# Kernel optimization log

Measured on AMD Instinct MI355X. Metric: run time of the kernel, lower is better.

The kernel has to match this reference:

```python
import jax, jax.numpy as jnp
import numpy as np

H = 768; NH = 8; DH = H // NH; MAXLEN = 512; EPS = 1e-5

def _sinusoid_pe():
    # get_embedding(max_seq_len, hidden, rel_pos_init=0): rows 0..2*max_len
    num = 2 * MAXLEN + 1
    half = H // 2
    inv = np.exp(np.arange(half, dtype=np.float64) * -(np.log(10000.0) / (half - 1)))
    ang = np.arange(num, dtype=np.float64)[:, None] * inv[None, :]
    return jnp.asarray(np.concatenate([np.sin(ang), np.cos(ang)], axis=1), jnp.float32)

def setup_inputs():
    key = jax.random.key(0)
    ks = jax.random.split(key, 20)
    B, S = 2, 192
    p = lambda k, shp: jax.random.normal(k, shp, jnp.float32) * 0.02
    z = lambda *shp: jnp.zeros(shp, jnp.float32)
    o = lambda *shp: jnp.ones(shp, jnp.float32)
    return dict(
        word_embedding=jax.random.normal(ks[0], (B, S, H), jnp.float32),
        bert_embedding=jax.random.normal(ks[1], (B, S, H), jnp.float32),
        seq_len=jax.random.randint(ks[2], (B,), 128, 161),
        lex_num=jax.random.randint(ks[3], (B,), 16, 32),
        pos_s=jax.random.randint(ks[4], (B, S), 0, 192),
        pos_e=jax.random.randint(ks[5], (B, S), 0, 192),
        pe=_sinusoid_pe(),
        Wf1=p(ks[6], (4 * H, 4 * H)), bf1=z(4 * H),
        Wf2=p(ks[7], (4 * H, 4)), bf2=z(4),
        Wq=p(ks[8], (H, H)), bq=z(H),
        Wk=p(ks[9], (H, H)), bk=z(H),
        Wv=p(ks[10], (H, H)), bv=z(H),
        Wr=p(ks[11], (H, H)), br=z(H),
        u=p(ks[12], (NH, DH)), v=p(ks[13], (NH, DH)),
        Wo=p(ks[14], (H, H)), bo=z(H),
        ln1_g=o(H), ln1_b=z(H),
        W1=p(ks[15], (H, H)), b1=z(H),
        W2=p(ks[16], (H, H)), b2=z(H),
        ln2_g=o(H), ln2_b=z(H),
    )

def _ln(x, g, b):
    m = jnp.mean(x, -1, keepdims=True)
    var = jnp.mean((x - m) ** 2, -1, keepdims=True)
    return (x - m) * jax.lax.rsqrt(var + EPS) * g + b

def reference(word_embedding, bert_embedding, seq_len, lex_num, pos_s, pos_e, pe,
              Wf1, bf1, Wf2, bf2, Wq, bq, Wk, bk, Wv, bv, Wr, br, u, v, Wo, bo,
              ln1_g, ln1_b, W1, b1, W2, b2, ln2_g, ln2_b):
    B, S, _ = word_embedding.shape
    x = bert_embedding + word_embedding  # [B,S,H]
    # --- four-way relative position fusion ('attn') ---
    dss = pos_s[:, :, None] - pos_s[:, None, :] + MAXLEN  # [B,S,S] in [0,2*MAXLEN]
    dse = pos_s[:, :, None] - pos_e[:, None, :] + MAXLEN
    des = pos_e[:, :, None] - pos_s[:, None, :] + MAXLEN
    dee = pos_e[:, :, None] - pos_e[:, None, :] + MAXLEN
    pe4 = jnp.concatenate([pe[dss], pe[dse], pe[des], pe[dee]], axis=-1)  # [B,S,S,4H]
    w4 = jax.nn.softmax(jax.nn.relu(pe4 @ Wf1 + bf1) @ Wf2 + bf2, axis=-1)  # [B,S,S,4]
    rel = jnp.einsum('bqkf,bqkfh->bqkh', w4, pe4.reshape(B, S, S, 4, H))  # [B,S,S,H]
    # --- lattice relative multi-head attention (Transformer-XL style A+C / B+D) ---
    q = (x @ Wq + bq).reshape(B, S, NH, DH)
    k = (x @ Wk + bk).reshape(B, S, NH, DH)
    vh = (x @ Wv + bv).reshape(B, S, NH, DH)
    r = (rel @ Wr + br).reshape(B, S, S, NH, DH)
    AC = jnp.einsum('bqnd,bknd->bnqk', q + u, k)
    BD = jnp.einsum('bqnd,bqknd->bnqk', q + v, r)
    att = (AC + BD) / np.sqrt(DH).astype(np.float32)  # scaled=True
    valid = jnp.arange(S)[None, :] < (seq_len + lex_num)[:, None]  # [B,S] key mask
    att = jnp.where(valid[:, None, None, :], att, jnp.float32(-1e15))
    pattn = jax.nn.softmax(att, axis=-1)
    ctx = jnp.einsum('bnqk,bknd->bqnd', pattn, vh).reshape(B, S, H)
    ctx = ctx @ Wo + bo  # attn_ff=True
    x = _ln(x + ctx, ln1_g, ln1_b)  # postprocess 'an'
    ff = jax.nn.relu(x @ W1 + b1) @ W2 + b2  # ff_size = hidden
    x = _ln(x + ff, ln2_g, ln2_b)
    return x[:, :256, :]
```

## Files before the change

kernel.cpp:

```cpp
#include <hip/hip_runtime.h>
#include <hip/hip_bf16.h>
#include <hip/hip_fp16.h>
#include <cstdint>

#define BB 2
#define SS 192
#define HH 768
#define NHH 8
#define DHH 96
#define H4 3072
#define NJ 383
#define NJP 384
#define JOFF 321
#define NPAIR 73728
#define ATT_SCALE 0.10206207261596575f

typedef _Float16 h2 __attribute__((ext_vector_type(2)));
typedef _Float16 h4v __attribute__((ext_vector_type(4)));
typedef _Float16 h8 __attribute__((ext_vector_type(8)));
typedef float f4 __attribute__((ext_vector_type(4)));

__global__ __launch_bounds__(256) void prep_kernel(
    const float4* __restrict__ we, const float4* __restrict__ be, float4* __restrict__ xb,
    const float* __restrict__ wf2, const float* __restrict__ bf1,
    const float* __restrict__ bq, const float* __restrict__ bk, const float* __restrict__ bv,
    h2* __restrict__ wf2pG, h2* __restrict__ bf1pG, float* __restrict__ bqkv,
    const float* __restrict__ s0, const float* __restrict__ s1, const float* __restrict__ s2,
    const float* __restrict__ s3, const float* __restrict__ s4, const float* __restrict__ s5,
    const float* __restrict__ s6, __half* __restrict__ BTsq,
    const float* __restrict__ Wf1, __half* __restrict__ BTf1) {
  __shared__ float tile[32][33];
  const int blk = blockIdx.x;
  const int t = threadIdx.x;
  if (blk < 288) {
    const int i = blk * 256 + t;
    float4 va = we[i], vb = be[i];
    xb[i] = make_float4(va.x + vb.x, va.y + vb.y, va.z + vb.z, va.w + vb.w);
  } else if (blk == 288) {
    for (int i = t; i < 6144; i += 256) {
      const int cw = i >> 2, f = i & 3;
      h2 v = {(_Float16)wf2[8 * cw + f], (_Float16)wf2[8 * cw + 4 + f]};
      wf2pG[i] = v;
    }
    for (int i = t; i < 1536; i += 256) {
      h2 v = {(_Float16)bf1[2 * i], (_Float16)bf1[2 * i + 1]};
      bf1pG[i] = v;
    }
    for (int i = t; i < 768; i += 256) {
      bqkv[i] = bq[i]; bqkv[768 + i] = bk[i]; bqkv[1536 + i] = bv[i];
    }
  } else if (blk < 4321) {
    const int i7 = blk - 289;
    const int z = i7 / 576, rem = i7 % 576;
    const int y = (rem / 24) * 32, x = (rem % 24) * 32;
    const float* src;
    switch (z) {
      case 0: src = s0; break; case 1: src = s1; break; case 2: src = s2; break;
      case 3: src = s3; break; case 4: src = s4; break; case 5: src = s5; break;
      default: src = s6; break;
    }
    __half* dst = BTsq + (size_t)z * HH * HH;
    const int tx = t & 31, ty = t >> 5;
#pragma unroll
    for (int i = 0; i < 4; ++i)
      tile[ty + 8 * i][tx] = src[(size_t)(y + ty + 8 * i) * HH + x + tx];
    __syncthreads();
#pragma unroll
    for (int i = 0; i < 4; ++i)
      dst[(size_t)(x + ty + 8 * i) * HH + y + tx] = __float2half(tile[tx][ty + 8 * i]);
  } else {
    const int ic = blk - 4321;
    const int z = ic / 2304, rem = ic % 2304;
    const int y = (rem / 96) * 32, x = (rem % 96) * 32;
    const float* src = Wf1 + (size_t)z * HH * H4;
    __half* dst = BTf1 + (size_t)z * HH * H4;
    const int tx = t & 31, ty = t >> 5;
#pragma unroll
    for (int i = 0; i < 4; ++i)
      tile[ty + 8 * i][tx] = src[(size_t)(y + ty + 8 * i) * H4 + x + tx];
    __syncthreads();
#pragma unroll
    for (int i = 0; i < 4; ++i)
      dst[(size_t)(x + ty + 8 * i) * HH + y + tx] = __float2half(tile[tx][ty + 8 * i]);
  }
}

template<bool OUT_HALF, bool RELU>
__device__ __forceinline__ void gemm_body(_Float16 (*As)[72], _Float16 (*Bs)[72],
    const float* __restrict__ A, const __half* __restrict__ Bb, const float* __restrict__ bias,
    void* __restrict__ Cv, int M, int N, int K, int bm, int bn, int t) {
  const int wave = t >> 6, lane = t & 63;
  const int wr = (wave >> 1) * 64, wc = (wave & 1) * 64;
  const int lrow = lane & 15, khalf = lane >> 4;
  const int arow = t >> 4, acol = (t & 15) << 2;
  const int brow = t >> 3, bcol = (t & 7) << 3;
  f4 acc[4][4] = {};
  const int nk = K >> 6;
  float4 ra[8]; h8 rb[4];

#define LOAD_TILE(kt) { \
  _Pragma("unroll") for (int i = 0; i < 8; ++i) { \
    const int row = arow + (i << 4); \
    if (bm + row < M) ra[i] = *(const float4*)(A + (size_t)(bm + row) * K + (size_t)(kt) * 64 + acol); \
    else ra[i] = make_float4(0.f, 0.f, 0.f, 0.f); } \
  _Pragma("unroll") for (int i = 0; i < 4; ++i) { \
    const int row = brow + (i << 5); \
    rb[i] = *(const h8*)(Bb + (size_t)(bn + row) * K + (size_t)(kt) * 64 + bcol); } }

#define STORE_TILE() { \
  _Pragma("unroll") for (int i = 0; i < 8; ++i) { \
    const int row = arow + (i << 4); \
    h4v hv = {(_Float16)ra[i].x, (_Float16)ra[i].y, (_Float16)ra[i].z, (_Float16)ra[i].w}; \
    *(h4v*)&As[row][acol] = hv; } \
  _Pragma("unroll") for (int i = 0; i < 4; ++i) { \
    const int row = brow + (i << 5); \
    *(h8*)&Bs[row][bcol] = rb[i]; } }

  LOAD_TILE(0)
  STORE_TILE()
  __syncthreads();
  for (int kt = 0; kt < nk; ++kt) {
    const bool more = (kt + 1 < nk);
    if (more) { LOAD_TILE(kt + 1) }
#pragma unroll
    for (int ks = 0; ks < 2; ++ks) {
      h8 af[4], bf[4];
#pragma unroll
      for (int mi = 0; mi < 4; ++mi) af[mi] = *(const h8*)&As[wr + mi * 16 + lrow][ks * 32 + (khalf << 3)];
#pragma unroll
      for (int ni = 0; ni < 4; ++ni) bf[ni] = *(const h8*)&Bs[wc + ni * 16 + lrow][ks * 32 + (khalf << 3)];
#pragma unroll
      for (int mi = 0; mi < 4; ++mi)
#pragma unroll
        for (int ni = 0; ni < 4; ++ni)
          acc[mi][ni] = __builtin_amdgcn_mfma_f32_16x16x32_f16(af[mi], bf[ni], acc[mi][ni], 0, 0, 0);
    }
    __syncthreads();
    if (more) { STORE_TILE() }
    __syncthreads();
  }
#undef LOAD_TILE
#undef STORE_TILE
  const int crow0 = (lane >> 4) << 2;
  const int ccol = lane & 15;
#pragma unroll
  for (int mi = 0; mi < 4; ++mi) {
#pragma unroll
    for (int r = 0; r < 4; ++r) {
      const int row = bm + wr + mi * 16 + crow0 + r;
      if (row >= M) continue;
#pragma unroll
      for (int ni = 0; ni < 4; ++ni) {
        const int col = bn + wc + ni * 16 + ccol;
        float v = acc[mi][ni][r];
        if (bias) v += bias[col];
        if (RELU) v = fmaxf(v, 0.f);
        if (OUT_HALF) ((__half*)Cv)[(size_t)row * N + col] = __float2half(v);
        else          ((float*)Cv)[(size_t)row * N + col] = v;
      }
    }
  }
}

template<bool OUT_HALF, bool RELU>
__global__ __launch_bounds__(256) void mfma_gemm(const float* __restrict__ A,
    const __half* __restrict__ BT, const float* __restrict__ bias, void* __restrict__ Cv,
    int M, int N, int K) {
  __shared__ _Float16 As[128][72];
  __shared__ _Float16 Bs[128][72];
  gemm_body<OUT_HALF, RELU>(As, Bs, A, BT, bias, Cv, M, N, K,
                            blockIdx.y * 128, blockIdx.x * 128, threadIdx.x);
}

__global__ __launch_bounds__(256) void gemm_batch(
    const float* __restrict__ peu, const __half* __restrict__ WrT, const float* __restrict__ br,
    float* __restrict__ PRb,
    const __half* __restrict__ BTf1, __half* __restrict__ Tt,
    const float* __restrict__ xb, const __half* __restrict__ BTsq, const float* __restrict__ bqkv,
    float* __restrict__ qkv) {
  __shared__ _Float16 As[128][72];
  __shared__ _Float16 Bs[128][72];
  const int blk = blockIdx.x;
  const int t = threadIdx.x;
  if (blk < 18) {
    gemm_body<false, false>(As, Bs, peu, WrT, br, PRb, NJ, HH, HH,
                            (blk / 6) * 128, (blk % 6) * 128, t);
  } else if (blk < 306) {
    const int i2 = blk - 18;
    const int z = i2 / 72, r = i2 % 72;
    gemm_body<true, false>(As, Bs, peu, BTf1 + (size_t)z * H4 * HH, nullptr,
                           Tt + (size_t)z * NJP * H4, NJ, H4, HH,
                           (r / 24) * 128, (r % 24) * 128, t);
  } else {
    const int i3 = blk - 306;
    gemm_body<false, false>(As, Bs, xb, BTsq, bqkv, qkv, BB * SS, 3 * HH, HH,
                            (i3 / 18) * 128, (i3 % 18) * 128, t);
  }
}

__global__ __launch_bounds__(256) void g2_kernel(const float* __restrict__ qkv,
    const float* __restrict__ PRb, const float* __restrict__ vv, float* __restrict__ G) {
  __shared__ float Qv[192][100];
  __shared__ float PRs[48][100];
  const int blk = blockIdx.x;
  const int jt = blk & 7, n = (blk >> 3) & 7, b = blk >> 6;
  const int j0 = jt * 48;
  const int t = threadIdx.x;
  for (int i = t; i < 4608; i += 256) {
    const int q = i / 24, c = (i % 24) * 4;
    float4 v = *(const float4*)(qkv + (size_t)(b * 192 + q) * 2304 + n * 96 + c);
    const float4 vb = *(const float4*)(vv + n * 96 + c);
    Qv[q][c] = v.x + vb.x; Qv[q][c + 1] = v.y + vb.y;
    Qv[q][c + 2] = v.z + vb.z; Qv[q][c + 3] = v.w + vb.w;
  }
  for (int i = t; i < 1152; i += 256) {
    const int jr = i / 24, c = (i % 24) * 4;
    const int j = min(j0 + jr, NJ - 1);
    *(f4*)&PRs[jr][c] = *(const f4*)(PRb + (size_t)j * 768 + n * 96 + c);
  }
  __syncthreads();
  const int qt = t >> 4, jt2 = t & 15;
  const int qb0 = qt * 12;
  float acc[12][3] = {};
  for (int dq = 0; dq < 24; ++dq) {
    const f4 p0 = *(const f4*)&PRs[jt2][dq * 4];
    const f4 p1 = *(const f4*)&PRs[jt2 + 16][dq * 4];
    const f4 p2 = *(const f4*)&PRs[jt2 + 32][dq * 4];
#pragma unroll
    for (int qi = 0; qi < 12; ++qi) {
      const f4 qv = *(const f4*)&Qv[qb0 + qi][dq * 4];
      acc[qi][0] += qv.x * p0.x + qv.y * p0.y + qv.z * p0.z + qv.w * p0.w;
      acc[qi][1] += qv.x * p1.x + qv.y * p1.y + qv.z * p1.z + qv.w * p1.w;
      acc[qi][2] += qv.x * p2.x + qv.y * p2.y + qv.z * p2.z + qv.w * p2.w;
    }
  }
  float* Grow = G + (size_t)(b * 8 + n) * 192 * NJP;
#pragma unroll
  for (int qi = 0; qi < 12; ++qi)
#pragma unroll
    for (int ji = 0; ji < 3; ++ji)
      Grow[(size_t)(qb0 + qi) * NJP + j0 + jt2 + 16 * ji] = acc[qi][ji];
}

__global__ __launch_bounds__(256) void pairA_kernel(const h2* __restrict__ Tt,
    const h8* __restrict__ wf2pG, const h2* __restrict__ bf1pG,
    const int* __restrict__ pos_s, const int* __restrict__ pos_e,
    float* __restrict__ partials) {
  const int blk = blockIdx.x;
  const int chunk = (blk & 7) >> 1;
  const int cbase = chunk * 384;
  const int t = threadIdx.x;
  const int grp = t >> 4, l16 = t & 15;
  const int pbase = (blk >> 3) * 128 + (blk & 1) * 64;
  const h2 zero2 = {(_Float16)0.f, (_Float16)0.f};
  h8 Wr[3][4]; h2 B1[3][4];
#pragma unroll
  for (int s = 0; s < 3; ++s)
#pragma unroll
    for (int v = 0; v < 4; ++v) {
      const int cw = (l16 + 16 * s) * 4 + v;
      Wr[s][v] = wf2pG[cbase + cw];
      B1[s][v] = bf1pG[cbase + cw];
    }
  const h2* Tc = Tt + cbase;
#pragma unroll 2
  for (int i = 0; i < 4; ++i) {
    const int p = pbase + i * 16 + grp;
    const int b = p / 36864;
    const int rem = p - b * 36864;
    const int qq = rem / 192;
    const int kk = rem - qq * 192;
    const int psq = pos_s[b * 192 + qq], peq = pos_e[b * 192 + qq];
    const int psk = pos_s[b * 192 + kk], pek = pos_e[b * 192 + kk];
    const int jx = min(max(psq - psk + 191, 0), NJ - 1);
    const int jy = min(max(psq - pek + 191, 0), NJ - 1);
    const int jz = min(max(peq - psk + 191, 0), NJ - 1);
    const int jw = min(max(peq - pek + 191, 0), NJ - 1);
    const h8* r0 = (const h8*)(Tc + (size_t)jx * 1536);
    const h8* r1 = (const h8*)(Tc + (size_t)(NJP + jy) * 1536);
    const h8* r2 = (const h8*)(Tc + (size_t)(2 * NJP + jz) * 1536);
    const h8* r3 = (const h8*)(Tc + (size_t)(3 * NJP + jw) * 1536);
    h2 c0 = zero2, c1 = zero2, c2 = zero2, c3 = zero2;
#pragma unroll
    for (int s = 0; s < 3; ++s) {
      const int g = l16 + 16 * s;
      union { h8 v; h2 p[4]; } L0, L1, L2, L3;
      L0.v = r0[g]; L1.v = r1[g]; L2.v = r2[g]; L3.v = r3[g];
#pragma unroll
      for (int v = 0; v < 4; ++v) {
        h2 sv = L0.p[v] + L1.p[v];
        sv = sv + L2.p[v];
        sv = sv + L3.p[v];
        sv = sv + B1[s][v];
        sv = __builtin_elementwise_max(sv, zero2);
        union { h8 v; h2 p[4]; } W; W.v = Wr[s][v];
        c0 += sv * W.p[0];
        c1 += sv * W.p[1];
        c2 += sv * W.p[2];
        c3 += sv * W.p[3];
      }
    }
    float a0 = (float)c0.x + (float)c0.y;
    float a1 = (float)c1.x + (float)c1.y;
    float a2 = (float)c2.x + (float)c2.y;
    float a3 = (float)c3.x + (float)c3.y;
#pragma unroll
    for (int off = 8; off > 0; off >>= 1) {
      a0 += __shfl_xor(a0, off, 16);
      a1 += __shfl_xor(a1, off, 16);
      a2 += __shfl_xor(a2, off, 16);
      a3 += __shfl_xor(a3, off, 16);
    }
    if (l16 < 4) {
      const float sel = (l16 == 0) ? a0 : (l16 == 1) ? a1 : (l16 == 2) ? a2 : a3;
      partials[((size_t)chunk * NPAIR + p) * 4 + l16] = sel;
    }
  }
}

__global__ __launch_bounds__(256) void attn2_kernel(const float* __restrict__ qkv,
    const float* __restrict__ uu, const float* __restrict__ G,
    const float4* __restrict__ parti4, const float* __restrict__ bf2,
    const int* __restrict__ pos_s, const int* __restrict__ pos_e,
    const int* __restrict__ seq_len, const int* __restrict__ lex_num,
    __half* __restrict__ P) {
  __shared__ float Ks[192][100];
  __shared__ float Qs[12][100];
  __shared__ float Gs[12][388];
  __shared__ int poss[192], pose[192];
  const int blk = blockIdx.x;
  const int qt = blk & 15, n = (blk >> 4) & 7, b = blk >> 7;
  const int q0 = qt * 12;
  const int t = threadIdx.x;
  for (int i = t; i < 4608; i += 256) {
    const int k = i / 24, c = (i % 24) * 4;
    *(f4*)&Ks[k][c] = *(const f4*)(qkv + (size_t)(b * 192 + k) * 2304 + 768 + n * 96 + c);
  }
  for (int i = t; i < 288; i += 256) {
    const int qi = i / 24, c = (i % 24) * 4;
    float4 v = *(const float4*)(qkv + (size_t)(b * 192 + q0 + qi) * 2304 + n * 96 + c);
    const float4 ub = *(const float4*)(uu + n * 96 + c);
    Qs[qi][c] = v.x + ub.x; Qs[qi][c + 1] = v.y + ub.y;
    Qs[qi][c + 2] = v.z + ub.z; Qs[qi][c + 3] = v.w + ub.w;
  }
  for (int i = t; i < 1152; i += 256) {
    const int qi = i / 96, c = (i % 96) * 4;
    *(f4*)&Gs[qi][c] = *(const f4*)(G + ((size_t)(b * 8 + n) * 192 + q0 + qi) * NJP + c);
  }
  for (int i = t; i < 192; i += 256) { poss[i] = pos_s[b * 192 + i]; pose[i] = pos_e[b * 192 + i]; }
  __syncthreads();
  const float b20 = bf2[0], b21 = bf2[1], b22 = bf2[2], b23 = bf2[3];
  const int wave = t >> 6, lane = t & 63;
  const int qw = wave * 3;
  float ac[3][3] = {};
  for (int dq = 0; dq < 24; ++dq) {
    const f4 kv0 = *(const f4*)&Ks[lane][dq * 4];
    const f4 kv1 = *(const f4*)&Ks[lane + 64][dq * 4];
    const f4 kv2 = *(const f4*)&Ks[lane + 128][dq * 4];
#pragma unroll
    for (int qi = 0; qi < 3; ++qi) {
      const f4 qv = *(const f4*)&Qs[qw + qi][dq * 4];
      ac[qi][0] += qv.x * kv0.x + qv.y * kv0.y + qv.z * kv0.z + qv.w * kv0.w;
      ac[qi][1] += qv.x * kv1.x + qv.y * kv1.y + qv.z * kv1.z + qv.w * kv1.w;
      ac[qi][2] += qv.x * kv2.x + qv.y * kv2.y + qv.z * kv2.z + qv.w * kv2.w;
    }
  }
  const int vbnd = seq_len[b] + lex_num[b];
#pragma unroll
  for (int qi = 0; qi < 3; ++qi) {
    const int qg = q0 + qw + qi;
    const int psq = poss[qg], peq = pose[qg];
    float v[3];
#pragma unroll
    for (int ki = 0; ki < 3; ++ki) {
      const int k = lane + 64 * ki;
      const int psk = poss[k], pek = pose[k];
      const int jss = min(max(psq - psk + 191, 0), NJ - 1);
      const int jse = min(max(psq - pek + 191, 0), NJ - 1);
      const int jes = min(max(peq - psk + 191, 0), NJ - 1);
      const int jee = min(max(peq - pek + 191, 0), NJ - 1);
      const int pidx = b * 36864 + qg * 192 + k;
      const float4 s0 = parti4[pidx];
      const float4 s1 = parti4[NPAIR + pidx];
      const float4 s2 = parti4[2 * NPAIR + pidx];
      const float4 s3 = parti4[3 * NPAIR + pidx];
      const float l0 = s0.x + s1.x + s2.x + s3.x + b20;
      const float l1 = s0.y + s1.y + s2.y + s3.y + b21;
      const float l2 = s0.z + s1.z + s2.z + s3.z + b22;
      const float l3 = s0.w + s1.w + s2.w + s3.w + b23;
      const float lm = fmaxf(fmaxf(l0, l1), fmaxf(l2, l3));
      const float e0 = __expf(l0 - lm), e1 = __expf(l1 - lm);
      const float e2 = __expf(l2 - lm), e3 = __expf(l3 - lm);
      const float winv = 1.f / (e0 + e1 + e2 + e3);
      const float bd = (e0 * Gs[qw + qi][jss] + e1 * Gs[qw + qi][jse]
                      + e2 * Gs[qw + qi][jes] + e3 * Gs[qw + qi][jee]) * winv;
      const float a = (ac[qi][ki] + bd) * ATT_SCALE;
      v[ki] = (k < vbnd) ? a : -1e15f;
    }
    float mx = fmaxf(fmaxf(v[0], v[1]), v[2]);
#pragma unroll
    for (int off = 1; off < 64; off <<= 1) mx = fmaxf(mx, __shfl_xor(mx, off, 64));
    const float e0 = __expf(v[0] - mx), e1 = __expf(v[1] - mx), e2 = __expf(v[2] - mx);
    float sm = e0 + e1 + e2;
#pragma unroll
    for (int off = 1; off < 64; off <<= 1) sm += __shfl_xor(sm, off, 64);
    const float inv = 1.f / sm;
    __half* pr = P + ((size_t)(b * 8 + n) * 192 + qg) * 192;
    pr[lane] = __float2half(e0 * inv);
    pr[lane + 64] = __float2half(e1 * inv);
    pr[lane + 128] = __float2half(e2 * inv);
  }
}

__global__ __launch_bounds__(256) void ctx2_kernel(const __half* __restrict__ P,
    const float* __restrict__ qkv, float* __restrict__ ctx) {
  __shared__ float Vs[192][100];
  __shared__ float Ps[48][196];
  const int blk = blockIdx.x;
  const int qt = blk & 3, n = (blk >> 2) & 7, b = blk >> 5;
  const int q0 = qt * 48;
  const int t = threadIdx.x;
  for (int i = t; i < 4608; i += 256) {
    const int k = i / 24, c = (i % 24) * 4;
    *(f4*)&Vs[k][c] = *(const f4*)(qkv + (size_t)(b * 192 + k) * 2304 + 1536 + n * 96 + c);
  }
  const __half* Pb = P + ((size_t)(b * 8 + n) * 192 + q0) * 192;
  for (int i = t; i < 4608; i += 256) {
    const int qi = i / 96, c = (i % 96) * 2;
    const h2 pv = *(const h2*)(Pb + (size_t)qi * 192 + c);
    Ps[qi][c] = (float)pv.x; Ps[qi][c + 1] = (float)pv.y;
  }
  __syncthreads();
  const int qt2 = t >> 5, dt = t & 31;
  const int qb0 = qt2 * 6;
  float acc[6][3] = {};
  for (int k4 = 0; k4 < 48; ++k4) {
    const int k = k4 * 4;
    f4 pq[6];
#pragma unroll
    for (int qi = 0; qi < 6; ++qi) pq[qi] = *(const f4*)&Ps[qb0 + qi][k];
#pragma unroll
    for (int kk = 0; kk < 4; ++kk) {
      const float v0 = Vs[k + kk][dt];
      const float v1 = Vs[k + kk][dt + 32];
      const float v2 = Vs[k + kk][dt + 64];
#pragma unroll
      for (int qi = 0; qi < 6; ++qi) {
        const float pv = pq[qi][kk];
        acc[qi][0] += pv * v0; acc[qi][1] += pv * v1; acc[qi][2] += pv * v2;
      }
    }
  }
#pragma unroll
  for (int qi = 0; qi < 6; ++qi) {
    float* cr = ctx + (size_t)(b * 192 + q0 + qb0 + qi) * 768 + n * 96;
    cr[dt] = acc[qi][0]; cr[dt + 32] = acc[qi][1]; cr[dt + 64] = acc[qi][2];
  }
}

__global__ __launch_bounds__(256) void ln_kernel(const float* __restrict__ xin,
    const float* __restrict__ dres, const float* __restrict__ g,
    const float* __restrict__ bta, float* __restrict__ out) {
  const int row = blockIdx.x;
  const int t = threadIdx.x;
  __shared__ float red[256];
  const size_t base = (size_t)row * HH;
  const float v0 = xin[base + t] + dres[base + t];
  const float v1 = xin[base + 256 + t] + dres[base + 256 + t];
  const float v2 = xin[base + 512 + t] + dres[base + 512 + t];
  red[t] = v0 + v1 + v2; __syncthreads();
  for (int s = 128; s > 0; s >>= 1) { if (t < s) red[t] += red[t + s]; __syncthreads(); }
  const float mean = red[0] * (1.f / 768.f); __syncthreads();
  red[t] = v0 * v0 + v1 * v1 + v2 * v2; __syncthreads();
  for (int s = 128; s > 0; s >>= 1) { if (t < s) red[t] += red[t + s]; __syncthreads(); }
  const float var = red[0] * (1.f / 768.f) - mean * mean;
  const float rstd = rsqrtf(var + 1e-5f);
  out[base + t]       = (v0 - mean) * rstd * g[t]       + bta[t];
  out[base + 256 + t] = (v1 - mean) * rstd * g[256 + t] + bta[256 + t];
  out[base + 512 + t] = (v2 - mean) * rstd * g[512 + t] + bta[512 + t];
}

extern "C" void kernel_launch(void* const* d_in, const int* in_sizes, int n_in,
                              void* d_out, int out_size, void* d_ws, size_t ws_size,
                              hipStream_t stream) {
  const float* we      = (const float*)d_in[0];
  const float* be      = (const float*)d_in[1];
  const int*   seq_len = (const int*)d_in[2];
  const int*   lex_num = (const int*)d_in[3];
  const int*   pos_s   = (const int*)d_in[4];
  const int*   pos_e   = (const int*)d_in[5];
  const float* pe      = (const float*)d_in[6];
  const float* Wf1     = (const float*)d_in[7];
  const float* bf1     = (const float*)d_in[8];
  const float* Wf2     = (const float*)d_in[9];
  const float* bf2     = (const float*)d_in[10];
  const float* Wq = (const float*)d_in[11]; const float* bq = (const float*)d_in[12];
  const float* Wk = (const float*)d_in[13]; const float* bk = (const float*)d_in[14];
  const float* Wv = (const float*)d_in[15]; const float* bv = (const float*)d_in[16];
  const float* Wr = (const float*)d_in[17]; const float* br = (const float*)d_in[18];
  const float* uu = (const float*)d_in[19]; const float* vv = (const float*)d_in[20];
  const float* Wo = (const float*)d_in[21]; const float* bo = (const float*)d_in[22];
  const float* g1 = (const float*)d_in[23]; const float* be1 = (const float*)d_in[24];
  const float* W1 = (const float*)d_in[25]; const float* b1 = (const float*)d_in[26];
  const float* W2 = (const float*)d_in[27]; const float* b2 = (const float*)d_in[28];
  const float* g2 = (const float*)d_in[29]; const float* be2 = (const float*)d_in[30];

  char* ws = (char*)d_ws;
  float*  xb    = (float*)(ws + 0);
  float*  qkv   = (float*)(ws + 1179648);
  float*  PRb   = (float*)(ws + 4718592);
  __half* Tt    = (__half*)(ws + 5898240);
  __half* BTf1  = (__half*)(ws + 15335424);
  float*  G     = (float*)(ws + 15335424);
  float*  parti = (float*)(ws + 20054016);
  __half* P     = (__half*)(ws + 25952256);
  float*  ctx   = (float*)(ws + 27131904);
  float*  ao    = (float*)(ws + 28311552);
  float*  x1    = (float*)(ws + 29491200);
  float*  ff    = (float*)(ws + 30670848);
  float*  fo    = (float*)(ws + 31850496);
  __half* BTsq  = (__half*)(ws + 34209792);
  h2*     wf2pG = (h2*)(ws + 42467328);
  h2*     bf1pG = (h2*)(ws + 42491904);
  float*  bqkv  = (float*)(ws + 42498048);
  float*  out   = (float*)d_out;

  const float* peu = pe + (size_t)JOFF * HH;
  const size_t SQ = (size_t)HH * HH;
  __half* WoT = BTsq + 3 * SQ; __half* W1T = BTsq + 4 * SQ;
  __half* W2T = BTsq + 5 * SQ; __half* WrT = BTsq + 6 * SQ;

  prep_kernel<<<13537, 256, 0, stream>>>((const float4*)we, (const float4*)be, (float4*)xb,
      Wf2, bf1, bq, bk, bv, wf2pG, bf1pG, bqkv,
      Wq, Wk, Wv, Wo, W1, W2, Wr, BTsq, Wf1, BTf1);
  gemm_batch<<<360, 256, 0, stream>>>(peu, WrT, br, PRb, BTf1, Tt, xb, BTsq, bqkv, qkv);
  g2_kernel<<<128, 256, 0, stream>>>(qkv, PRb, vv, G);
  pairA_kernel<<<4608, 256, 0, stream>>>((const h2*)Tt, (const h8*)wf2pG, bf1pG,
      pos_s, pos_e, parti);
  attn2_kernel<<<256, 256, 0, stream>>>(qkv, uu, G, (const float4*)parti, bf2,
      pos_s, pos_e, seq_len, lex_num, P);
  ctx2_kernel<<<64, 256, 0, stream>>>(P, qkv, ctx);
  mfma_gemm<false, false><<<dim3(6, 3), 256, 0, stream>>>(ctx, WoT, bo, ao, BB * SS, HH, HH);
  ln_kernel<<<BB * SS, 256, 0, stream>>>(xb, ao, g1, be1, x1);
  mfma_gemm<false, true><<<dim3(6, 3), 256, 0, stream>>>(x1, W1T, b1, ff, BB * SS, HH, HH);
  mfma_gemm<false, false><<<dim3(6, 3), 256, 0, stream>>>(ff, W2T, b2, fo, BB * SS, HH, HH);
  ln_kernel<<<BB * SS, 256, 0, stream>>>(x1, fo, g2, be2, out);
}
```

Measured before the change: 405.7 us.

## Widen GEMM blocks to 8 waves and split attention/context kernels finer

```diff
diff --git a/kernel.cpp b/kernel.cpp
--- a/kernel.cpp
+++ b/kernel.cpp
@@ -90,30 +90,30 @@
     const float* __restrict__ A, const __half* __restrict__ Bb, const float* __restrict__ bias,
     void* __restrict__ Cv, int M, int N, int K, int bm, int bn, int t) {
   const int wave = t >> 6, lane = t & 63;
-  const int wr = (wave >> 1) * 64, wc = (wave & 1) * 64;
+  const int wr = (wave >> 2) * 64, wc = (wave & 3) * 32;
   const int lrow = lane & 15, khalf = lane >> 4;
   const int arow = t >> 4, acol = (t & 15) << 2;
   const int brow = t >> 3, bcol = (t & 7) << 3;
-  f4 acc[4][4] = {};
+  f4 acc[4][2] = {};
   const int nk = K >> 6;
-  float4 ra[8]; h8 rb[4];
+  float4 ra[4]; h8 rb[2];
 
 #define LOAD_TILE(kt) { \
-  _Pragma("unroll") for (int i = 0; i < 8; ++i) { \
-    const int row = arow + (i << 4); \
+  _Pragma("unroll") for (int i = 0; i < 4; ++i) { \
+    const int row = arow + (i << 5); \
     if (bm + row < M) ra[i] = *(const float4*)(A + (size_t)(bm + row) * K + (size_t)(kt) * 64 + acol); \
     else ra[i] = make_float4(0.f, 0.f, 0.f, 0.f); } \
+  _Pragma("unroll") for (int i = 0; i < 2; ++i) { \
+    const int row = brow + (i << 6); \
+    rb[i] = *(const h8*)(Bb + (size_t)(bn + row) * K + (size_t)(kt) * 64 + bcol); } }
+
+#define STORE_TILE() { \
   _Pragma("unroll") for (int i = 0; i < 4; ++i) { \
-    const int row = brow + (i << 5); \
-    rb[i] = *(const h8*)(Bb + (size_t)(bn + row) * K + (size_t)(kt) * 64 + bcol); } }
-
-#define STORE_TILE() { \
-  _Pragma("unroll") for (int i = 0; i < 8; ++i) { \
-    const int row = arow + (i << 4); \
+    const int row = arow + (i << 5); \
     h4v hv = {(_Float16)ra[i].x, (_Float16)ra[i].y, (_Float16)ra[i].z, (_Float16)ra[i].w}; \
     *(h4v*)&As[row][acol] = hv; } \
-  _Pragma("unroll") for (int i = 0; i < 4; ++i) { \
-    const int row = brow + (i << 5); \
+  _Pragma("unroll") for (int i = 0; i < 2; ++i) { \
+    const int row = brow + (i << 6); \
     *(h8*)&Bs[row][bcol] = rb[i]; } }
 
   LOAD_TILE(0)
@@ -124,15 +124,15 @@
     if (more) { LOAD_TILE(kt + 1) }
 #pragma unroll
     for (int ks = 0; ks < 2; ++ks) {
-      h8 af[4], bf[4];
+      h8 af[4], bf[2];
 #pragma unroll
       for (int mi = 0; mi < 4; ++mi) af[mi] = *(const h8*)&As[wr + mi * 16 + lrow][ks * 32 + (khalf << 3)];
 #pragma unroll
-      for (int ni = 0; ni < 4; ++ni) bf[ni] = *(const h8*)&Bs[wc + ni * 16 + lrow][ks * 32 + (khalf << 3)];
+      for (int ni = 0; ni < 2; ++ni) bf[ni] = *(const h8*)&Bs[wc + ni * 16 + lrow][ks * 32 + (khalf << 3)];
 #pragma unroll
       for (int mi = 0; mi < 4; ++mi)
 #pragma unroll
-        for (int ni = 0; ni < 4; ++ni)
+        for (int ni = 0; ni < 2; ++ni)
           acc[mi][ni] = __builtin_amdgcn_mfma_f32_16x16x32_f16(af[mi], bf[ni], acc[mi][ni], 0, 0, 0);
     }
     __syncthreads();
@@ -150,7 +150,7 @@
       const int row = bm + wr + mi * 16 + crow0 + r;
       if (row >= M) continue;
 #pragma unroll
-      for (int ni = 0; ni < 4; ++ni) {
+      for (int ni = 0; ni < 2; ++ni) {
         const int col = bn + wc + ni * 16 + ccol;
         float v = acc[mi][ni][r];
         if (bias) v += bias[col];
@@ -163,7 +163,7 @@
 }
 
 template<bool OUT_HALF, bool RELU>
-__global__ __launch_bounds__(256) void mfma_gemm(const float* __restrict__ A,
+__global__ __launch_bounds__(512) void mfma_gemm(const float* __restrict__ A,
     const __half* __restrict__ BT, const float* __restrict__ bias, void* __restrict__ Cv,
     int M, int N, int K) {
   __shared__ _Float16 As[128][72];
@@ -172,7 +172,7 @@
                             blockIdx.y * 128, blockIdx.x * 128, threadIdx.x);
 }
 
-__global__ __launch_bounds__(256) void gemm_batch(
+__global__ __launch_bounds__(512) void gemm_batch(
     const float* __restrict__ peu, const __half* __restrict__ WrT, const float* __restrict__ br,
     float* __restrict__ PRb,
     const __half* __restrict__ BTf1, __half* __restrict__ Tt,
@@ -318,144 +318,129 @@
   }
 }
 
-__global__ __launch_bounds__(256) void attn2_kernel(const float* __restrict__ qkv,
+__global__ __launch_bounds__(384) void attn3_kernel(const float* __restrict__ qkv,
     const float* __restrict__ uu, const float* __restrict__ G,
     const float4* __restrict__ parti4, const float* __restrict__ bf2,
     const int* __restrict__ pos_s, const int* __restrict__ pos_e,
     const int* __restrict__ seq_len, const int* __restrict__ lex_num,
     __half* __restrict__ P) {
-  __shared__ float Ks[192][100];
-  __shared__ float Qs[12][100];
-  __shared__ float Gs[12][388];
+  __shared__ _Float16 Kh[192][100];
+  __shared__ float Qs[6][100];
+  __shared__ float Gs[6][388];
   __shared__ int poss[192], pose[192];
   const int blk = blockIdx.x;
-  const int qt = blk & 15, n = (blk >> 4) & 7, b = blk >> 7;
-  const int q0 = qt * 12;
-  const int t = threadIdx.x;
-  for (int i = t; i < 4608; i += 256) {
+  const int qt = blk & 31, n = (blk >> 5) & 7, b = blk >> 8;
+  const int q0 = qt * 6;
+  const int t = threadIdx.x;
+  for (int i = t; i < 4608; i += 384) {
     const int k = i / 24, c = (i % 24) * 4;
-    *(f4*)&Ks[k][c] = *(const f4*)(qkv + (size_t)(b * 192 + k) * 2304 + 768 + n * 96 + c);
-  }
-  for (int i = t; i < 288; i += 256) {
-    const int qi = i / 24, c = (i % 24) * 4;
+    const float4 v = *(const float4*)(qkv + (size_t)(b * 192 + k) * 2304 + 768 + n * 96 + c);
+    h4v hv = {(_Float16)v.x, (_Float16)v.y, (_Float16)v.z, (_Float16)v.w};
+    *(h4v*)&Kh[k][c] = hv;
+  }
+  if (t < 144) {
+    const int qi = t / 24, c = (t % 24) * 4;
     float4 v = *(const float4*)(qkv + (size_t)(b * 192 + q0 + qi) * 2304 + n * 96 + c);
     const float4 ub = *(const float4*)(uu + n * 96 + c);
     Qs[qi][c] = v.x + ub.x; Qs[qi][c + 1] = v.y + ub.y;
     Qs[qi][c + 2] = v.z + ub.z; Qs[qi][c + 3] = v.w + ub.w;
   }
-  for (int i = t; i < 1152; i += 256) {
+  for (int i = t; i < 576; i += 384) {
     const int qi = i / 96, c = (i % 96) * 4;
     *(f4*)&Gs[qi][c] = *(const f4*)(G + ((size_t)(b * 8 + n) * 192 + q0 + qi) * NJP + c);
   }
-  for (int i = t; i < 192; i += 256) { poss[i] = pos_s[b * 192 + i]; pose[i] = pos_e[b * 192 + i]; }
+  for (int i = t; i < 192; i += 384) { poss[i] = pos_s[b * 192 + i]; pose[i] = pos_e[b * 192 + i]; }
   __syncthreads();
   const float b20 = bf2[0], b21 = bf2[1], b22 = bf2[2], b23 = bf2[3];
   const int wave = t >> 6, lane = t & 63;
-  const int qw = wave * 3;
-  float ac[3][3] = {};
+  float ac0 = 0.f, ac1 = 0.f, ac2 = 0.f;
   for (int dq = 0; dq < 24; ++dq) {
-    const f4 kv0 = *(const f4*)&Ks[lane][dq * 4];
-    const f4 kv1 = *(const f4*)&Ks[lane + 64][dq * 4];
-    const f4 kv2 = *(const f4*)&Ks[lane + 128][dq * 4];
-#pragma unroll
-    for (int qi = 0; qi < 3; ++qi) {
-      const f4 qv = *(const f4*)&Qs[qw + qi][dq * 4];
-      ac[qi][0] += qv.x * kv0.x + qv.y * kv0.y + qv.z * kv0.z + qv.w * kv0.w;
-      ac[qi][1] += qv.x * kv1.x + qv.y * kv1.y + qv.z * kv1.z + qv.w * kv1.w;
-      ac[qi][2] += qv.x * kv2.x + qv.y * kv2.y + qv.z * kv2.z + qv.w * kv2.w;
-    }
+    const f4 qv = *(const f4*)&Qs[wave][dq * 4];
+    const h4v k0 = *(const h4v*)&Kh[lane][dq * 4];
+    const h4v k1 = *(const h4v*)&Kh[lane + 64][dq * 4];
+    const h4v k2 = *(const h4v*)&Kh[lane + 128][dq * 4];
+    ac0 += qv.x * (float)k0.x + qv.y * (float)k0.y + qv.z * (float)k0.z + qv.w * (float)k0.w;
+    ac1 += qv.x * (float)k1.x + qv.y * (float)k1.y + qv.z * (float)k1.z + qv.w * (float)k1.w;
+    ac2 += qv.x * (float)k2.x + qv.y * (float)k2.y + qv.z * (float)k2.z + qv.w * (float)k2.w;
   }
   const int vbnd = seq_len[b] + lex_num[b];
-#pragma unroll
-  for (int qi = 0; qi < 3; ++qi) {
-    const int qg = q0 + qw + qi;
-    const int psq = poss[qg], peq = pose[qg];
-    float v[3];
-#pragma unroll
-    for (int ki = 0; ki < 3; ++ki) {
-      const int k = lane + 64 * ki;
-      const int psk = poss[k], pek = pose[k];
-      const int jss = min(max(psq - psk + 191, 0), NJ - 1);
-      const int jse = min(max(psq - pek + 191, 0), NJ - 1);
-      const int jes = min(max(peq - psk + 191, 0), NJ - 1);
-      const int jee = min(max(peq - pek + 191, 0), NJ - 1);
-      const int pidx = b * 36864 + qg * 192 + k;
-      const float4 s0 = parti4[pidx];
-      const float4 s1 = parti4[NPAIR + pidx];
-      const float4 s2 = parti4[2 * NPAIR + pidx];
-      const float4 s3 = parti4[3 * NPAIR + pidx];
-      const float l0 = s0.x + s1.x + s2.x + s3.x + b20;
-      const float l1 = s0.y + s1.y + s2.y + s3.y + b21;
-      const float l2 = s0.z + s1.z + s2.z + s3.z + b22;
-      const float l3 = s0.w + s1.w + s2.w + s3.w + b23;
-      const float lm = fmaxf(fmaxf(l0, l1), fmaxf(l2, l3));
-      const float e0 = __expf(l0 - lm), e1 = __expf(l1 - lm);
-      const float e2 = __expf(l2 - lm), e3 = __expf(l3 - lm);
-      const float winv = 1.f / (e0 + e1 + e2 + e3);
-      const float bd = (e0 * Gs[qw + qi][jss] + e1 * Gs[qw + qi][jse]
-                      + e2 * Gs[qw + qi][jes] + e3 * Gs[qw + qi][jee]) * winv;
-      const float a = (ac[qi][ki] + bd) * ATT_SCALE;
-      v[ki] = (k < vbnd) ? a : -1e15f;
-    }
-    float mx = fmaxf(fmaxf(v[0], v[1]), v[2]);
-#pragma unroll
-    for (int off = 1; off < 64; off <<= 1) mx = fmaxf(mx, __shfl_xor(mx, off, 64));
-    const float e0 = __expf(v[0] - mx), e1 = __expf(v[1] - mx), e2 = __expf(v[2] - mx);
-    float sm = e0 + e1 + e2;
-#pragma unroll
-    for (int off = 1; off < 64; off <<= 1) sm += __shfl_xor(sm, off, 64);
-    const float inv = 1.f / sm;
-    __half* pr = P + ((size_t)(b * 8 + n) * 192 + qg) * 192;
-    pr[lane] = __float2half(e0 * inv);
-    pr[lane + 64] = __float2half(e1 * inv);
-    pr[lane + 128] = __float2half(e2 * inv);
-  }
-}
-
-__global__ __launch_bounds__(256) void ctx2_kernel(const __half* __restrict__ P,
+  const int qg = q0 + wave;
+  const int psq = poss[qg], peq = pose[qg];
+  float v[3];
+  const float acv[3] = {ac0, ac1, ac2};
+#pragma unroll
+  for (int ki = 0; ki < 3; ++ki) {
+    const int k = lane + 64 * ki;
+    const int psk = poss[k], pek = pose[k];
+    const int jss = min(max(psq - psk + 191, 0), NJ - 1);
+    const int jse = min(max(psq - pek + 191, 0), NJ - 1);
+    const int jes = min(max(peq - psk + 191, 0), NJ - 1);
+    const int jee = min(max(peq - pek + 191, 0), NJ - 1);
+    const int pidx = b * 36864 + qg * 192 + k;
+    const float4 s0 = parti4[pidx];
+    const float4 s1 = parti4[NPAIR + pidx];
+    const float4 s2 = parti4[2 * NPAIR + pidx];
+    const float4 s3 = parti4[3 * NPAIR + pidx];
+    const float l0 = s0.x + s1.x + s2.x + s3.x + b20;
+    const float l1 = s0.y + s1.y + s2.y + s3.y + b21;
+    const float l2 = s0.z + s1.z + s2.z + s3.z + b22;
+    const float l3 = s0.w + s1.w + s2.w + s3.w + b23;
+    const float lm = fmaxf(fmaxf(l0, l1), fmaxf(l2, l3));
+    const float e0 = __expf(l0 - lm), e1 = __expf(l1 - lm);
+    const float e2 = __expf(l2 - lm), e3 = __expf(l3 - lm);
+    const float winv = 1.f / (e0 + e1 + e2 + e3);
+    const float bd = (e0 * Gs[wave][jss] + e1 * Gs[wave][jse]
+                    + e2 * Gs[wave][jes] + e3 * Gs[wave][jee]) * winv;
+    const float a = (acv[ki] + bd) * ATT_SCALE;
+    v[ki] = (k < vbnd) ? a : -1e15f;
+  }
+  float mx = fmaxf(fmaxf(v[0], v[1]), v[2]);
+#pragma unroll
+  for (int off = 1; off < 64; off <<= 1) mx = fmaxf(mx, __shfl_xor(mx, off, 64));
+  const float e0 = __expf(v[0] - mx), e1 = __expf(v[1] - mx), e2 = __expf(v[2] - mx);
+  float sm = e0 + e1 + e2;
+#pragma unroll
+  for (int off = 1; off < 64; off <<= 1) sm += __shfl_xor(sm, off, 64);
+  const float inv = 1.f / sm;
+  __half* pr = P + ((size_t)(b * 8 + n) * 192 + qg) * 192;
+  pr[lane] = __float2half(e0 * inv);
+  pr[lane + 64] = __float2half(e1 * inv);
+  pr[lane + 128] = __float2half(e2 * inv);
+}
+
+__global__ __launch_bounds__(384) void ctx3_kernel(const __half* __restrict__ P,
     const float* __restrict__ qkv, float* __restrict__ ctx) {
-  __shared__ float Vs[192][100];
-  __shared__ float Ps[48][196];
+  __shared__ _Float16 Vh[192][100];
+  __shared__ float Ps[12][192];
   const int blk = blockIdx.x;
-  const int qt = blk & 3, n = (blk >> 2) & 7, b = blk >> 5;
-  const int q0 = qt * 48;
-  const int t = threadIdx.x;
-  for (int i = t; i < 4608; i += 256) {
+  const int qt = blk & 15, n = (blk >> 4) & 7, b = blk >> 7;
+  const int q0 = qt * 12;
+  const int t = threadIdx.x;
+  for (int i = t; i < 4608; i += 384) {
     const int k = i / 24, c = (i % 24) * 4;
-    *(f4*)&Vs[k][c] = *(const f4*)(qkv + (size_t)(b * 192 + k) * 2304 + 1536 + n * 96 + c);
+    const float4 v = *(const float4*)(qkv + (size_t)(b * 192 + k) * 2304 + 1536 + n * 96 + c);
+    h4v hv = {(_Float16)v.x, (_Float16)v.y, (_Float16)v.z, (_Float16)v.w};
+    *(h4v*)&Vh[k][c] = hv;
   }
   const __half* Pb = P + ((size_t)(b * 8 + n) * 192 + q0) * 192;
-  for (int i = t; i < 4608; i += 256) {
+  for (int i = t; i < 1152; i += 384) {
     const int qi = i / 96, c = (i % 96) * 2;
     const h2 pv = *(const h2*)(Pb + (size_t)qi * 192 + c);
     Ps[qi][c] = (float)pv.x; Ps[qi][c + 1] = (float)pv.y;
   }
   __syncthreads();
-  const int qt2 = t >> 5, dt = t & 31;
-  const int qb0 = qt2 * 6;
-  float acc[6][3] = {};
-  for (int k4 = 0; k4 < 48; ++k4) {
-    const int k = k4 * 4;
-    f4 pq[6];
-#pragma unroll
-    for (int qi = 0; qi < 6; ++qi) pq[qi] = *(const f4*)&Ps[qb0 + qi][k];
-#pragma unroll
-    for (int kk = 0; kk < 4; ++kk) {
-      const float v0 = Vs[k + kk][dt];
-      const float v1 = Vs[k + kk][dt + 32];
-      const float v2 = Vs[k + kk][dt + 64];
-#pragma unroll
-      for (int qi = 0; qi < 6; ++qi) {
-        const float pv = pq[qi][kk];
-        acc[qi][0] += pv * v0; acc[qi][1] += pv * v1; acc[qi][2] += pv * v2;
-      }
-    }
-  }
-#pragma unroll
-  for (int qi = 0; qi < 6; ++qi) {
-    float* cr = ctx + (size_t)(b * 192 + q0 + qb0 + qi) * 768 + n * 96;
-    cr[dt] = acc[qi][0]; cr[dt + 32] = acc[qi][1]; cr[dt + 64] = acc[qi][2];
-  }
+  const int d = t % 96, qg = t / 96;
+  const int qb0 = qg * 3;
+  float a0 = 0.f, a1 = 0.f, a2 = 0.f;
+#pragma unroll 4
+  for (int k = 0; k < 192; ++k) {
+    const float vv = (float)Vh[k][d];
+    a0 += Ps[qb0 + 0][k] * vv;
+    a1 += Ps[qb0 + 1][k] * vv;
+    a2 += Ps[qb0 + 2][k] * vv;
+  }
+  float* cr = ctx + (size_t)(b * 192 + q0 + qb0) * 768 + n * 96 + d;
+  cr[0] = a0; cr[768] = a1; cr[1536] = a2;
 }
 
 __global__ __launch_bounds__(256) void ln_kernel(const float* __restrict__ xin,
@@ -533,16 +518,16 @@
   prep_kernel<<<13537, 256, 0, stream>>>((const float4*)we, (const float4*)be, (float4*)xb,
       Wf2, bf1, bq, bk, bv, wf2pG, bf1pG, bqkv,
       Wq, Wk, Wv, Wo, W1, W2, Wr, BTsq, Wf1, BTf1);
-  gemm_batch<<<360, 256, 0, stream>>>(peu, WrT, br, PRb, BTf1, Tt, xb, BTsq, bqkv, qkv);
+  gemm_batch<<<360, 512, 0, stream>>>(peu, WrT, br, PRb, BTf1, Tt, xb, BTsq, bqkv, qkv);
   g2_kernel<<<128, 256, 0, stream>>>(qkv, PRb, vv, G);
   pairA_kernel<<<4608, 256, 0, stream>>>((const h2*)Tt, (const h8*)wf2pG, bf1pG,
       pos_s, pos_e, parti);
-  attn2_kernel<<<256, 256, 0, stream>>>(qkv, uu, G, (const float4*)parti, bf2,
+  attn3_kernel<<<512, 384, 0, stream>>>(qkv, uu, G, (const float4*)parti, bf2,
       pos_s, pos_e, seq_len, lex_num, P);
-  ctx2_kernel<<<64, 256, 0, stream>>>(P, qkv, ctx);
-  mfma_gemm<false, false><<<dim3(6, 3), 256, 0, stream>>>(ctx, WoT, bo, ao, BB * SS, HH, HH);
+  ctx3_kernel<<<256, 384, 0, stream>>>(P, qkv, ctx);
+  mfma_gemm<false, false><<<dim3(6, 3), 512, 0, stream>>>(ctx, WoT, bo, ao, BB * SS, HH, HH);
   ln_kernel<<<BB * SS, 256, 0, stream>>>(xb, ao, g1, be1, x1);
-  mfma_gemm<false, true><<<dim3(6, 3), 256, 0, stream>>>(x1, W1T, b1, ff, BB * SS, HH, HH);
-  mfma_gemm<false, false><<<dim3(6, 3), 256, 0, stream>>>(ff, W2T, b2, fo, BB * SS, HH, HH);
+  mfma_gemm<false, true><<<dim3(6, 3), 512, 0, stream>>>(x1, W1T, b1, ff, BB * SS, HH, HH);
+  mfma_gemm<false, false><<<dim3(6, 3), 512, 0, stream>>>(ff, W2T, b2, fo, BB * SS, HH, HH);
   ln_kernel<<<BB * SS, 256, 0, stream>>>(x1, fo, g2, be2, out);
 }
```

Measured after the change: 344.3 us. 15.2% less time.
